# Performance work log

Hardware: AMD Instinct MI355X
Metric: run time of the kernel (lower is better)

The kernel has to match this reference:

```python
import jax, jax.numpy as jnp
import numpy as np

B, C, H, W = 8, 512, 64, 64
NUMS, V_C = 1024, 512
RATE = 0.999


def _normalize(x):
    # matches torch F.normalize(dim=-1, eps=1e-12)
    return x / jnp.clip(jnp.linalg.norm(x, axis=-1, keepdims=True), 1e-12)


def setup_inputs() -> dict:
    key = jax.random.key(0)
    k1, k2, k3 = jax.random.split(key, 3)
    return {
        "x": jax.random.normal(k1, (B, C, H, W), dtype=jnp.float32),
        "noise_feature": jax.random.normal(k2, (NUMS, C), dtype=jnp.float32),
        "std": jax.random.normal(k3, (NUMS, V_C), dtype=jnp.float32),
    }


def reference(x, noise_feature, std):
    b, c, h, w = x.shape
    # (b,c,h,w) -> (n,c)
    xf = jnp.transpose(x, (0, 2, 3, 1)).reshape(-1, c)
    m = jax.lax.stop_gradient(noise_feature)  # torch uses .data (no grad)
    xn = _normalize(xf)
    mn = _normalize(m)
    score = xn @ mn.T  # (n, k) cosine similarities

    # EMA codebook update (training path, update_flag=True)
    xd = jax.lax.stop_gradient(xf)
    embed_ind = jnp.argmax(score, axis=1)  # (n,)
    # segment_sum == x.T @ one_hot(ind), transposed; avoids dense one-hot GEMM
    embed_sum = jax.ops.segment_sum(xd, embed_ind, num_segments=NUMS)  # (k, c)
    counts = jax.ops.segment_sum(jnp.ones((xd.shape[0],), xd.dtype), embed_ind,
                                 num_segments=NUMS)  # (k,)
    embed_mean = embed_sum / (counts[:, None] + 1e-6)
    new_m = m * RATE + embed_mean * (1.0 - RATE)

    mn2 = _normalize(new_m)
    score2 = xn @ mn2.T  # (n, k)
    soft_label = jax.nn.softmax(score2, axis=1)
    out = (soft_label @ std).reshape(b, h, w, V_C)
    return out, score2
```

## Files before the change

kernel.cpp:

```cpp
#include <hip/hip_runtime.h>
#include <stdint.h>

#define NROWS 32768
#define CDIM  512
#define KCODES 1024
#define VC    512
#define LDP 72

typedef unsigned short u16;
typedef unsigned long long u64;
using bf16x8 = __attribute__((ext_vector_type(8))) __bf16;
using f32x4  = __attribute__((ext_vector_type(4))) float;

__device__ __forceinline__ float bf2f(u16 u){
  union { unsigned int i; float f; } x; x.i = ((unsigned int)u) << 16; return x.f;
}
__device__ __forceinline__ u16 f2bf(float f){
  union { float f; unsigned int i; } x; x.f = f;
  unsigned int u = x.i;
  u += 0x7fffu + ((u >> 16) & 1u);
  return (u16)(u >> 16);
}
__device__ __forceinline__ unsigned int pack2(u16 lo, u16 hi){
  return (unsigned int)lo | ((unsigned int)hi << 16);
}
__device__ __forceinline__ unsigned int fkey(float f){
  unsigned int u = __float_as_uint(f);
  return (u & 0x80000000u) ? ~u : (u | 0x80000000u);
}
__device__ __forceinline__ f32x4 mfma16(bf16x8 a, bf16x8 b, f32x4 c){
  return __builtin_amdgcn_mfma_f32_16x16x32_bf16(a, b, c, 0, 0, 0);
}
__device__ __forceinline__ void gload_lds16(const void* g, void* l){
  __builtin_amdgcn_global_load_lds(
      (const __attribute__((address_space(1))) unsigned int*)g,
      (__attribute__((address_space(3))) unsigned int*)l, 16, 0, 0);
}

__global__ __launch_bounds__(256) void k_transpose_x(const float* __restrict__ x,
                                                     u16* __restrict__ xf,
                                                     float* __restrict__ rsum){
  __shared__ float tile[64 * 64];
  int b  = blockIdx.z;
  int p0 = blockIdx.x * 64;
  int c0 = blockIdx.y * 64;
  int t  = threadIdx.x;
  const float* xb = x + (size_t)b * CDIM * 4096 + (size_t)c0 * 4096 + p0;

  int pl4 = (t & 15) * 4;
#pragma unroll
  for (int i = 0; i < 4; i++){
    int cl = i * 16 + (t >> 4);
    float4 v = *(const float4*)(xb + (size_t)cl * 4096 + pl4);
    *(float4*)(tile + cl * 64 + (pl4 ^ (cl & 0x38))) = v;
  }
  __syncthreads();

  int cl0 = (t & 7) * 8;
#pragma unroll
  for (int pass = 0; pass < 2; pass++){
    int pl = pass * 32 + (t >> 3);
    float v[8]; float s = 0.f;
#pragma unroll
    for (int j = 0; j < 8; j++){
      v[j] = tile[(cl0 + j) * 64 + (pl ^ cl0)];
      s += v[j] * v[j];
    }
    uint4 o;
    o.x = pack2(f2bf(v[0]), f2bf(v[1]));
    o.y = pack2(f2bf(v[2]), f2bf(v[3]));
    o.z = pack2(f2bf(v[4]), f2bf(v[5]));
    o.w = pack2(f2bf(v[6]), f2bf(v[7]));
    *(uint4*)(xf + (size_t)(b * 4096 + p0 + pl) * CDIM + c0 + cl0) = o;
    s += __shfl_xor(s, 1, 64);
    s += __shfl_xor(s, 2, 64);
    s += __shfl_xor(s, 4, 64);
    if ((t & 7) == 0) atomicAdd(rsum + b * 4096 + p0 + pl, s);
  }
}

__global__ __launch_bounds__(256) void k_prep(const float* __restrict__ in,
                                              u16* __restrict__ mn,
                                              const float* __restrict__ sd,
                                              u16* __restrict__ stdT){
  int t = threadIdx.x;
  if (blockIdx.x < 256){
    int row  = blockIdx.x * 4 + (t >> 6);
    int lane = t & 63;
    const float* r = in + (size_t)row * CDIM;
    float v[8]; float s = 0.f;
#pragma unroll
    for (int i = 0; i < 8; i++){ v[i] = r[lane + i * 64]; s += v[i] * v[i]; }
#pragma unroll
    for (int off = 32; off; off >>= 1) s += __shfl_xor(s, off, 64);
    float inv = 1.0f / fmaxf(sqrtf(s), 1e-12f);
#pragma unroll
    for (int i = 0; i < 8; i++) mn[(size_t)row * CDIM + lane + i * 64] = f2bf(v[i] * inv);
  } else {
    __shared__ float tile[32][33];
    int bid = blockIdx.x - 256;
    int k0 = (bid & 31) * 32;
    int v0 = (bid >> 5) * 32;
    int tx = t & 31, ty = t >> 5;
#pragma unroll
    for (int i = 0; i < 4; i++)
      tile[ty + i * 8][tx] = sd[(size_t)(k0 + ty + i * 8) * VC + v0 + tx];
    __syncthreads();
#pragma unroll
    for (int i = 0; i < 4; i++)
      stdT[(size_t)(v0 + ty + i * 8) * KCODES + k0 + tx] = f2bf(tile[tx][ty + i * 8]);
  }
}

__global__ __launch_bounds__(256) void k_gemm1_am(const u16* __restrict__ xf,
                                                  const u16* __restrict__ mn,
                                                  u64* __restrict__ packed){
  __shared__ __align__(16) u16 As[128 * 64];
  __shared__ __align__(16) u16 Bs[128 * 64];
  int tid  = threadIdx.x;
  int wave = tid >> 6, lane = tid & 63;
  int wr = wave >> 1, wc = wave & 1;
  int quad = lane >> 4, l15 = lane & 15;
  int c0 = blockIdx.x * 128, r0 = blockIdx.y * 128;

  int srow = lane >> 3, schunk = lane & 7;
  const u16* ag = xf + (size_t)(r0 + wave * 8 + srow) * CDIM + schunk * 8;
  const u16* bg = mn + (size_t)(c0 + wave * 8 + srow) * CDIM + schunk * 8;
  u16* adst = As + wave * 8 * 64;
  u16* bdst = Bs + wave * 8 * 64;

  f32x4 acc[4][4];
#pragma unroll
  for (int rt = 0; rt < 4; rt++)
#pragma unroll
    for (int ct = 0; ct < 4; ct++) acc[rt][ct] = (f32x4)(0.f);

  for (int k0 = 0; k0 < CDIM; k0 += 64){
#pragma unroll
    for (int i = 0; i < 4; i++){
      gload_lds16(ag + (size_t)i * 32 * CDIM + k0, adst + i * 32 * 64);
      gload_lds16(bg + (size_t)i * 32 * CDIM + k0, bdst + i * 32 * 64);
    }
    __syncthreads();
#pragma unroll
    for (int ks = 0; ks < 2; ks++){
      bf16x8 af[4], bfr[4];
#pragma unroll
      for (int rt = 0; rt < 4; rt++)
        af[rt] = *(const bf16x8*)(As + (wr * 64 + rt * 16 + l15) * 64 + ks * 32 + quad * 8);
#pragma unroll
      for (int ct = 0; ct < 4; ct++)
        bfr[ct] = *(const bf16x8*)(Bs + (wc * 64 + ct * 16 + l15) * 64 + ks * 32 + quad * 8);
#pragma unroll
      for (int rt = 0; rt < 4; rt++)
#pragma unroll
        for (int ct = 0; ct < 4; ct++)
          acc[rt][ct] = mfma16(af[rt], bfr[ct], acc[rt][ct]);
    }
    __syncthreads();
  }

#pragma unroll
  for (int rt = 0; rt < 4; rt++){
#pragma unroll
    for (int q = 0; q < 4; q++){
      float bv = acc[rt][0][q];
      int   bc = c0 + wc * 64 + l15;
#pragma unroll
      for (int ct = 1; ct < 4; ct++){
        float v = acc[rt][ct][q];
        int   c = c0 + wc * 64 + ct * 16 + l15;
        if (v > bv){ bv = v; bc = c; }
      }
#pragma unroll
      for (int off = 1; off <= 8; off <<= 1){
        float ov = __shfl_xor(bv, off, 64);
        int   oc = __shfl_xor(bc, off, 64);
        if (ov > bv || (ov == bv && oc < bc)){ bv = ov; bc = oc; }
      }
      if (l15 == 0){
        int rg = r0 + wr * 64 + rt * 16 + quad * 4 + q;
        u64 key = ((u64)fkey(bv) << 32) | (unsigned int)(~(unsigned int)bc);
        atomicMax(packed + rg, key);
      }
    }
  }
}

__global__ __launch_bounds__(256) void k_gather(const u64* __restrict__ packed,
                                                const u16* __restrict__ xf,
                                                float* __restrict__ esum,
                                                float* __restrict__ counts){
  __shared__ float part[4][CDIM];
  __shared__ int   wcnt[4];
  int code = blockIdx.x;
  int tid = threadIdx.x, wave = tid >> 6, lane = tid & 63;
  float acc[8] = {0,0,0,0,0,0,0,0};
  int cnt = 0;
  for (int base = wave * 64; base < NROWS; base += 256){
    u64 pk = packed[base + lane];
    int cl = (int)(~(unsigned int)(pk & 0xffffffffull)) & (KCODES - 1);
    int match = (cl == code);
    u64 mask = __ballot(match);
    cnt += (int)__popcll(mask);
    while (mask){
      int b = __ffsll((long long)mask) - 1;
      mask &= mask - 1;
      int rr = base + b;
      uint4 v = *(const uint4*)(xf + (size_t)rr * CDIM + lane * 8);
      unsigned int w[4] = {v.x, v.y, v.z, v.w};
#pragma unroll
      for (int i = 0; i < 4; i++){
        acc[2 * i]     += bf2f((u16)(w[i] & 0xffffu));
        acc[2 * i + 1] += bf2f((u16)(w[i] >> 16));
      }
    }
  }
#pragma unroll
  for (int j = 0; j < 8; j++) part[wave][lane * 8 + j] = acc[j];
  if (lane == 0) wcnt[wave] = cnt;
  __syncthreads();
  for (int c = tid; c < CDIM; c += 256)
    esum[(size_t)code * CDIM + c] = part[0][c] + part[1][c] + part[2][c] + part[3][c];
  if (tid == 0) counts[code] = (float)(wcnt[0] + wcnt[1] + wcnt[2] + wcnt[3]);
}

__global__ __launch_bounds__(256) void k_newm(const float* __restrict__ m,
                                              const float* __restrict__ esum,
                                              const float* __restrict__ counts,
                                              u16* __restrict__ mn2){
  int row  = blockIdx.x * 4 + (threadIdx.x >> 6);
  int lane = threadIdx.x & 63;
  float cnt = counts[row];
  float sc  = 0.001f / (cnt + 1e-6f);
  float v[8]; float s = 0.f;
#pragma unroll
  for (int i = 0; i < 8; i++){
    int c = lane + i * 64;
    v[i] = m[(size_t)row * CDIM + c] * 0.999f + esum[(size_t)row * CDIM + c] * sc;
    s += v[i] * v[i];
  }
#pragma unroll
  for (int off = 32; off; off >>= 1) s += __shfl_xor(s, off, 64);
  float inv = 1.0f / fmaxf(sqrtf(s), 1e-12f);
#pragma unroll
  for (int i = 0; i < 8; i++) mn2[(size_t)row * CDIM + lane + i * 64] = f2bf(v[i] * inv);
}

__global__ __launch_bounds__(256) void k_gemm2(const u16* __restrict__ xf,
                                               const u16* __restrict__ mn2,
                                               const float* __restrict__ rsum,
                                               float* __restrict__ score2,
                                               float* __restrict__ pmax,
                                               float* __restrict__ psum){
  __shared__ __align__(16) u16 As[128 * 64];
  __shared__ __align__(16) u16 Bs[128 * 64];
  int tid  = threadIdx.x;
  int wave = tid >> 6, lane = tid & 63;
  int wr = wave >> 1, wc = wave & 1;
  int quad = lane >> 4, l15 = lane & 15;
  int c0 = blockIdx.x * 128, r0 = blockIdx.y * 128;

  int srow = lane >> 3, schunk = lane & 7;
  const u16* ag = xf  + (size_t)(r0 + wave * 8 + srow) * CDIM + schunk * 8;
  const u16* bg = mn2 + (size_t)(c0 + wave * 8 + srow) * CDIM + schunk * 8;
  u16* adst = As + wave * 8 * 64;
  u16* bdst = Bs + wave * 8 * 64;

  f32x4 acc[4][4];
#pragma unroll
  for (int rt = 0; rt < 4; rt++)
#pragma unroll
    for (int ct = 0; ct < 4; ct++) acc[rt][ct] = (f32x4)(0.f);

  for (int k0 = 0; k0 < CDIM; k0 += 64){
#pragma unroll
    for (int i = 0; i < 4; i++){
      gload_lds16(ag + (size_t)i * 32 * CDIM + k0, adst + i * 32 * 64);
      gload_lds16(bg + (size_t)i * 32 * CDIM + k0, bdst + i * 32 * 64);
    }
    __syncthreads();
#pragma unroll
    for (int ks = 0; ks < 2; ks++){
      bf16x8 af[4], bfr[4];
#pragma unroll
      for (int rt = 0; rt < 4; rt++)
        af[rt] = *(const bf16x8*)(As + (wr * 64 + rt * 16 + l15) * 64 + ks * 32 + quad * 8);
#pragma unroll
      for (int ct = 0; ct < 4; ct++)
        bfr[ct] = *(const bf16x8*)(Bs + (wc * 64 + ct * 16 + l15) * 64 + ks * 32 + quad * 8);
#pragma unroll
      for (int rt = 0; rt < 4; rt++)
#pragma unroll
        for (int ct = 0; ct < 4; ct++)
          acc[rt][ct] = mfma16(af[rt], bfr[ct], acc[rt][ct]);
    }
    __syncthreads();
  }

#pragma unroll
  for (int rt = 0; rt < 4; rt++){
#pragma unroll
    for (int q = 0; q < 4; q++){
      int grow = r0 + wr * 64 + rt * 16 + quad * 4 + q;
      float rv = 1.0f / fmaxf(sqrtf(rsum[grow]), 1e-12f);
      float v0 = acc[rt][0][q] * rv;
      float v1 = acc[rt][1][q] * rv;
      float v2 = acc[rt][2][q] * rv;
      float v3 = acc[rt][3][q] * rv;
      float* so = score2 + (size_t)grow * KCODES + c0 + wc * 64 + l15;
      so[0]  = v0;
      so[16] = v1;
      so[32] = v2;
      so[48] = v3;
      float mx = fmaxf(fmaxf(v0, v1), fmaxf(v2, v3));
#pragma unroll
      for (int off = 1; off <= 8; off <<= 1) mx = fmaxf(mx, __shfl_xor(mx, off, 64));
      float s = __expf(v0 - mx) + __expf(v1 - mx) + __expf(v2 - mx) + __expf(v3 - mx);
#pragma unroll
      for (int off = 1; off <= 8; off <<= 1) s += __shfl_xor(s, off, 64);
      if (l15 == 0){
        int pi = grow * 16 + blockIdx.x * 2 + wc;
        pmax[pi] = mx;
        psum[pi] = s;
      }
    }
  }
}

__global__ __launch_bounds__(256) void k_softcomb(const float* __restrict__ pmax,
                                                  const float* __restrict__ psum,
                                                  float* __restrict__ rowmax,
                                                  float* __restrict__ rsinv){
  int row = blockIdx.x * 256 + threadIdx.x;
  const float* pm = pmax + (size_t)row * 16;
  const float* ps = psum + (size_t)row * 16;
  float M = pm[0];
#pragma unroll
  for (int i = 1; i < 16; i++) M = fmaxf(M, pm[i]);
  float S = 0.f;
#pragma unroll
  for (int i = 0; i < 16; i++) S += ps[i] * __expf(pm[i] - M);
  rowmax[row] = M;
  rsinv[row]  = 1.0f / S;
}

__global__ __launch_bounds__(512) void k_gemm3(const float* __restrict__ score2,
                                               const float* __restrict__ rowmax,
                                               const float* __restrict__ rsinv,
                                               const u16* __restrict__ stdT,
                                               float* __restrict__ out){
  __shared__ __align__(16) u16 As[128 * LDP];
  __shared__ __align__(16) u16 Bs[512 * 64];
  int tid  = threadIdx.x;
  int wave = tid >> 6, lane = tid & 63;
  int wr = wave >> 2, wcol = wave & 3;
  int quad = lane >> 4, l15 = lane & 15;
  int r0 = blockIdx.x * 128;
  int arow = tid >> 2, aq = tid & 3;

  int srow = lane >> 3, schunk = lane & 7;
  const u16* bg = stdT + (size_t)(wave * 8 + srow) * KCODES + schunk * 8;
  u16* bdst = Bs + wave * 8 * 64;

  float rmax = rowmax[r0 + arow];
  float rs   = rsinv [r0 + arow];

  f32x4 acc[4][8];
#pragma unroll
  for (int rt = 0; rt < 4; rt++)
#pragma unroll
    for (int ct = 0; ct < 8; ct++) acc[rt][ct] = (f32x4)(0.f);

  const float* ag = score2 + (size_t)(r0 + arow) * KCODES + aq * 16;

  for (int k0 = 0; k0 < KCODES; k0 += 64){
#pragma unroll
    for (int i = 0; i < 8; i++)
      gload_lds16(bg + (size_t)i * 64 * KCODES + k0, bdst + i * 64 * 64);
#pragma unroll
    for (int j = 0; j < 2; j++){
      float4 a = *(const float4*)(ag + k0 + j * 8);
      float4 b = *(const float4*)(ag + k0 + j * 8 + 4);
      uint4 o;
      o.x = pack2(f2bf(__expf(a.x - rmax) * rs), f2bf(__expf(a.y - rmax) * rs));
      o.y = pack2(f2bf(__expf(a.z - rmax) * rs), f2bf(__expf(a.w - rmax) * rs));
      o.z = pack2(f2bf(__expf(b.x - rmax) * rs), f2bf(__expf(b.y - rmax) * rs));
      o.w = pack2(f2bf(__expf(b.z - rmax) * rs), f2bf(__expf(b.w - rmax) * rs));
      *(uint4*)(As + arow * LDP + aq * 16 + j * 8) = o;
    }
    __syncthreads();
#pragma unroll
    for (int ks = 0; ks < 2; ks++){
      bf16x8 af[4];
#pragma unroll
      for (int rt = 0; rt < 4; rt++)
        af[rt] = *(const bf16x8*)(As + (wr * 64 + rt * 16 + l15) * LDP + ks * 32 + quad * 8);
#pragma unroll
      for (int ct = 0; ct < 8; ct++){
        bf16x8 bv = *(const bf16x8*)(Bs + (wcol * 128 + ct * 16 + l15) * 64 + ks * 32 + quad * 8);
#pragma unroll
        for (int rt = 0; rt < 4; rt++)
          acc[rt][ct] = mfma16(af[rt], bv, acc[rt][ct]);
      }
    }
    __syncthreads();
  }
#pragma unroll
  for (int rt = 0; rt < 4; rt++){
#pragma unroll
    for (int q = 0; q < 4; q++){
      int grow = r0 + wr * 64 + rt * 16 + quad * 4 + q;
#pragma unroll
      for (int ct = 0; ct < 8; ct++){
        int gcol = wcol * 128 + ct * 16 + l15;
        out[(size_t)grow * VC + gcol] = acc[rt][ct][q];
      }
    }
  }
}

extern "C" void kernel_launch(void* const* d_in, const int* in_sizes, int n_in,
                              void* d_out, int out_size, void* d_ws, size_t ws_size,
                              hipStream_t stream){
  (void)in_sizes; (void)n_in; (void)out_size; (void)ws_size;
  const float* x      = (const float*)d_in[0];
  const float* m      = (const float*)d_in[1];
  const float* stdmat = (const float*)d_in[2];
  float* out    = (float*)d_out;
  float* score2 = out + (size_t)NROWS * VC;

  char* ws = (char*)d_ws;
  u16*   xf     = (u16*)  (ws + 0);
  u16*   mn     = (u16*)  (ws + 33554432);
  u16*   mn2    = (u16*)  (ws + 34603008);
  u16*   stdT   = (u16*)  (ws + 35651584);
  u64*   packed = (u64*)  (ws + 36831232);
  float* esum   = (float*)(ws + 37224448);
  float* counts = (float*)(ws + 39321600);
  float* rowmax = (float*)(ws + 39325696);
  float* rsinv  = (float*)(ws + 39456768);
  float* pmax   = (float*)(ws + 39587840);
  float* psum   = (float*)(ws + 41684992);
  float* rsum   = rowmax;

  hipMemsetAsync(packed, 0, (size_t)NROWS * 8, stream);
  hipMemsetAsync(rsum,   0, (size_t)NROWS * 4, stream);

  k_transpose_x  <<<dim3(64, 8, 8), 256, 0, stream>>>(x, xf, rsum);
  k_prep         <<<768, 256, 0, stream>>>(m, mn, stdmat, stdT);
  k_gemm1_am     <<<dim3(KCODES / 128, NROWS / 128), 256, 0, stream>>>(xf, mn, packed);
  k_gather       <<<KCODES, 256, 0, stream>>>(packed, xf, esum, counts);
  k_newm         <<<KCODES / 4, 256, 0, stream>>>(m, esum, counts, mn2);
  k_gemm2        <<<dim3(KCODES / 128, NROWS / 128), 256, 0, stream>>>(xf, mn2, rsum, score2, pmax, psum);
  k_softcomb     <<<NROWS / 256, 256, 0, stream>>>(pmax, psum, rowmax, rsinv);
  k_gemm3        <<<NROWS / 128, 512, 0, stream>>>(score2, rowmax, rsinv, stdT, out);
}
```

Measured before the change: 514.1 us.

## Retile GEMM kernels: 256-row blocks for gemm1/gemm2, split gemm3 columns

gemm1 and gemm2 now use 512-thread blocks covering 256 rows by 128 codes, so each loaded codebook tile is reused across twice as many rows and B-tile global traffic per output drops. gemm3 is split into two column halves of 256 output channels on a 2D grid. This doubles its block count and shrinks per-block LDS and accumulator registers, which aims for better occupancy. In exchange, the softmax exp/convert of score2 is now done twice per row, once in each column block, and score2 is read twice.

Measured after the change: 463.2 us. -9.9%, faster.

```diff
diff --git a/kernel.cpp b/kernel.cpp
--- a/kernel.cpp
+++ b/kernel.cpp
@@ -112,16 +112,16 @@
   }
 }
 
-__global__ __launch_bounds__(256) void k_gemm1_am(const u16* __restrict__ xf,
-                                                  const u16* __restrict__ mn,
-                                                  u64* __restrict__ packed){
-  __shared__ __align__(16) u16 As[128 * 64];
+__global__ __launch_bounds__(512, 4) void k_gemm1_am(const u16* __restrict__ xf,
+                                                     const u16* __restrict__ mn,
+                                                     u64* __restrict__ packed){
+  __shared__ __align__(16) u16 As[256 * 64];
   __shared__ __align__(16) u16 Bs[128 * 64];
   int tid  = threadIdx.x;
   int wave = tid >> 6, lane = tid & 63;
   int wr = wave >> 1, wc = wave & 1;
   int quad = lane >> 4, l15 = lane & 15;
-  int c0 = blockIdx.x * 128, r0 = blockIdx.y * 128;
+  int c0 = blockIdx.x * 128, r0 = blockIdx.y * 256;
 
   int srow = lane >> 3, schunk = lane & 7;
   const u16* ag = xf + (size_t)(r0 + wave * 8 + srow) * CDIM + schunk * 8;
@@ -137,10 +137,11 @@
 
   for (int k0 = 0; k0 < CDIM; k0 += 64){
 #pragma unroll
-    for (int i = 0; i < 4; i++){
-      gload_lds16(ag + (size_t)i * 32 * CDIM + k0, adst + i * 32 * 64);
-      gload_lds16(bg + (size_t)i * 32 * CDIM + k0, bdst + i * 32 * 64);
-    }
+    for (int i = 0; i < 4; i++)
+      gload_lds16(ag + (size_t)(i * 64) * CDIM + k0, adst + i * 64 * 64);
+#pragma unroll
+    for (int j = 0; j < 2; j++)
+      gload_lds16(bg + (size_t)(j * 64) * CDIM + k0, bdst + j * 64 * 64);
     __syncthreads();
 #pragma unroll
     for (int ks = 0; ks < 2; ks++){
@@ -247,19 +248,19 @@
   for (int i = 0; i < 8; i++) mn2[(size_t)row * CDIM + lane + i * 64] = f2bf(v[i] * inv);
 }
 
-__global__ __launch_bounds__(256) void k_gemm2(const u16* __restrict__ xf,
-                                               const u16* __restrict__ mn2,
-                                               const float* __restrict__ rsum,
-                                               float* __restrict__ score2,
-                                               float* __restrict__ pmax,
-                                               float* __restrict__ psum){
-  __shared__ __align__(16) u16 As[128 * 64];
+__global__ __launch_bounds__(512, 4) void k_gemm2(const u16* __restrict__ xf,
+                                                  const u16* __restrict__ mn2,
+                                                  const float* __restrict__ rsum,
+                                                  float* __restrict__ score2,
+                                                  float* __restrict__ pmax,
+                                                  float* __restrict__ psum){
+  __shared__ __align__(16) u16 As[256 * 64];
   __shared__ __align__(16) u16 Bs[128 * 64];
   int tid  = threadIdx.x;
   int wave = tid >> 6, lane = tid & 63;
   int wr = wave >> 1, wc = wave & 1;
   int quad = lane >> 4, l15 = lane & 15;
-  int c0 = blockIdx.x * 128, r0 = blockIdx.y * 128;
+  int c0 = blockIdx.x * 128, r0 = blockIdx.y * 256;
 
   int srow = lane >> 3, schunk = lane & 7;
   const u16* ag = xf  + (size_t)(r0 + wave * 8 + srow) * CDIM + schunk * 8;
@@ -275,10 +276,11 @@
 
   for (int k0 = 0; k0 < CDIM; k0 += 64){
 #pragma unroll
-    for (int i = 0; i < 4; i++){
-      gload_lds16(ag + (size_t)i * 32 * CDIM + k0, adst + i * 32 * 64);
-      gload_lds16(bg + (size_t)i * 32 * CDIM + k0, bdst + i * 32 * 64);
-    }
+    for (int i = 0; i < 4; i++)
+      gload_lds16(ag + (size_t)(i * 64) * CDIM + k0, adst + i * 64 * 64);
+#pragma unroll
+    for (int j = 0; j < 2; j++)
+      gload_lds16(bg + (size_t)(j * 64) * CDIM + k0, bdst + j * 64 * 64);
     __syncthreads();
 #pragma unroll
     for (int ks = 0; ks < 2; ks++){
@@ -351,32 +353,32 @@
                                                const u16* __restrict__ stdT,
                                                float* __restrict__ out){
   __shared__ __align__(16) u16 As[128 * LDP];
-  __shared__ __align__(16) u16 Bs[512 * 64];
+  __shared__ __align__(16) u16 Bs[256 * 64];
   int tid  = threadIdx.x;
   int wave = tid >> 6, lane = tid & 63;
   int wr = wave >> 2, wcol = wave & 3;
   int quad = lane >> 4, l15 = lane & 15;
-  int r0 = blockIdx.x * 128;
+  int c0 = blockIdx.x * 256, r0 = blockIdx.y * 128;
   int arow = tid >> 2, aq = tid & 3;
 
   int srow = lane >> 3, schunk = lane & 7;
-  const u16* bg = stdT + (size_t)(wave * 8 + srow) * KCODES + schunk * 8;
+  const u16* bg = stdT + (size_t)(c0 + wave * 8 + srow) * KCODES + schunk * 8;
   u16* bdst = Bs + wave * 8 * 64;
 
   float rmax = rowmax[r0 + arow];
   float rs   = rsinv [r0 + arow];
 
-  f32x4 acc[4][8];
+  f32x4 acc[4][4];
 #pragma unroll
   for (int rt = 0; rt < 4; rt++)
 #pragma unroll
-    for (int ct = 0; ct < 8; ct++) acc[rt][ct] = (f32x4)(0.f);
+    for (int ct = 0; ct < 4; ct++) acc[rt][ct] = (f32x4)(0.f);
 
   const float* ag = score2 + (size_t)(r0 + arow) * KCODES + aq * 16;
 
   for (int k0 = 0; k0 < KCODES; k0 += 64){
 #pragma unroll
-    for (int i = 0; i < 8; i++)
+    for (int i = 0; i < 4; i++)
       gload_lds16(bg + (size_t)i * 64 * KCODES + k0, bdst + i * 64 * 64);
 #pragma unroll
     for (int j = 0; j < 2; j++){
@@ -392,17 +394,18 @@
     __syncthreads();
 #pragma unroll
     for (int ks = 0; ks < 2; ks++){
-      bf16x8 af[4];
+      bf16x8 af[4], bfr[4];
 #pragma unroll
       for (int rt = 0; rt < 4; rt++)
         af[rt] = *(const bf16x8*)(As + (wr * 64 + rt * 16 + l15) * LDP + ks * 32 + quad * 8);
 #pragma unroll
-      for (int ct = 0; ct < 8; ct++){
-        bf16x8 bv = *(const bf16x8*)(Bs + (wcol * 128 + ct * 16 + l15) * 64 + ks * 32 + quad * 8);
-#pragma unroll
-        for (int rt = 0; rt < 4; rt++)
-          acc[rt][ct] = mfma16(af[rt], bv, acc[rt][ct]);
-      }
+      for (int ct = 0; ct < 4; ct++)
+        bfr[ct] = *(const bf16x8*)(Bs + (wcol * 64 + ct * 16 + l15) * 64 + ks * 32 + quad * 8);
+#pragma unroll
+      for (int rt = 0; rt < 4; rt++)
+#pragma unroll
+        for (int ct = 0; ct < 4; ct++)
+          acc[rt][ct] = mfma16(af[rt], bfr[ct], acc[rt][ct]);
     }
     __syncthreads();
   }
@@ -412,8 +415,8 @@
     for (int q = 0; q < 4; q++){
       int grow = r0 + wr * 64 + rt * 16 + quad * 4 + q;
 #pragma unroll
-      for (int ct = 0; ct < 8; ct++){
-        int gcol = wcol * 128 + ct * 16 + l15;
+      for (int ct = 0; ct < 4; ct++){
+        int gcol = c0 + wcol * 64 + ct * 16 + l15;
         out[(size_t)grow * VC + gcol] = acc[rt][ct][q];
       }
     }
@@ -449,10 +452,10 @@
 
   k_transpose_x  <<<dim3(64, 8, 8), 256, 0, stream>>>(x, xf, rsum);
   k_prep         <<<768, 256, 0, stream>>>(m, mn, stdmat, stdT);
-  k_gemm1_am     <<<dim3(KCODES / 128, NROWS / 128), 256, 0, stream>>>(xf, mn, packed);
+  k_gemm1_am     <<<dim3(KCODES / 128, NROWS / 256), 512, 0, stream>>>(xf, mn, packed);
   k_gather       <<<KCODES, 256, 0, stream>>>(packed, xf, esum, counts);
   k_newm         <<<KCODES / 4, 256, 0, stream>>>(m, esum, counts, mn2);
-  k_gemm2        <<<dim3(KCODES / 128, NROWS / 128), 256, 0, stream>>>(xf, mn2, rsum, score2, pmax, psum);
+  k_gemm2        <<<dim3(KCODES / 128, NROWS / 256), 512, 0, stream>>>(xf, mn2, rsum, score2, pmax, psum);
   k_softcomb     <<<NROWS / 256, 256, 0, stream>>>(pmax, psum, rowmax, rsinv);
-  k_gemm3        <<<NROWS / 128, 512, 0, stream>>>(score2, rowmax, rsinv, stdT, out);
-}
+  k_gemm3        <<<dim3(VC / 256, NROWS / 128), 512, 0, stream>>>(score2, rowmax, rsinv, stdT, out);
+}
```
